# Optimization experiments

Hardware: AMD Instinct MI355X
Metric: run time of the kernel (lower is better)

The kernel has to match this reference:

```python
import jax, jax.numpy as jnp
import numpy as np

TOP_K = 2
ROUTED_SCALING = 1.0


def setup_inputs() -> dict:
    key = jax.random.key(0)
    k1, k2, k3, k4 = jax.random.split(key, 4)
    S, B, H = 1024, 2, 1024
    E, FFN = 8, 1408
    return {
        "hidden_states": jax.random.normal(k1, (S, B, H), dtype=jnp.float32),
        "gate_w": jax.random.normal(k2, (E, H), dtype=jnp.float32) * 0.02,
        "w1": jax.random.normal(k3, (E, H, 2 * FFN), dtype=jnp.float32) * 0.02,
        "w2": jax.random.normal(k4, (E, FFN, H), dtype=jnp.float32) * 0.02,
    }


def reference(hidden_states, gate_w, w1, w2):
    # hidden_states: [S, B, H] -> transpose(0,1) as in MoELayer.forward
    x = jnp.transpose(hidden_states, (1, 0, 2))  # [B, S, H]
    B, S, H = x.shape
    E = gate_w.shape[0]
    xt = x.reshape(-1, H)  # [T, H], T = B*S
    T = xt.shape[0]

    # --- TopKGate ('greedy', softmax scoring) ---
    scores = jax.nn.softmax(xt @ gate_w.T, axis=-1)  # [T, E]
    topk_w, topk_idx = jax.lax.top_k(scores, TOP_K)  # [T, K]
    # norm_topk_prob: normalize the top-k weights
    topk_w = topk_w / (jnp.sum(topk_w, axis=-1, keepdims=True) + 1e-20)
    topk_w = topk_w * ROUTED_SCALING

    # Sparse combine weights [T, E] (zero for non-selected experts)
    combine = jnp.zeros((T, E), dtype=xt.dtype)
    combine = combine.at[jnp.arange(T)[:, None], topk_idx].set(topk_w)

    # --- Experts: per-expert swiglu MLP, weighted combine ---
    # Equivalent math to dispatch -> per-expert grouped GEMM -> combine:
    # non-selected experts contribute with weight 0.
    out = jnp.zeros_like(xt)
    for e in range(E):
        h = xt @ w1[e]                      # [T, 2*FFN]
        g, u = jnp.split(h, 2, axis=-1)
        y = (jax.nn.silu(g) * u) @ w2[e]    # [T, H]
        out = out + combine[:, e:e + 1] * y

    out = out.reshape(B, S, H)
    return jnp.transpose(out, (1, 0, 2))  # back to [S, B, H]
```

## Files before the change

### kernel.cpp

```cpp
#include <hip/hip_runtime.h>
#include <hip/hip_bf16.h>

#define S_      1024
#define B_      2
#define H_      1024
#define E_      8
#define FFN_    1408
#define TWO_FFN 2816
#define T_      2048
#define MAXSLOTS 5120
#define NB_T1   (44 * 16 * 8)
#define NB_T2   (16 * 22 * 8)
#define NB_CONV 512
#define NB_PREP (NB_T1 + NB_T2 + NB_CONV)

typedef float  f32x4 __attribute__((ext_vector_type(4)));
typedef short  s16x8 __attribute__((ext_vector_type(8)));

__device__ __forceinline__ unsigned short f2bf(float f) {
    unsigned u = __float_as_uint(f);
    u += 0x7fffu + ((u >> 16) & 1u);
    return (unsigned short)(u >> 16);
}
__device__ __forceinline__ void async16(const void* g, void* l) {
    __builtin_amdgcn_global_load_lds(
        (const __attribute__((address_space(1))) unsigned int*)(unsigned long long)g,
        (__attribute__((address_space(3))) unsigned int*)(unsigned long long)l,
        16, 0, 0);
}
__device__ __forceinline__ size_t xrow_off(int t) {
    return (size_t)(t & (S_ - 1)) * (B_ * H_) + (size_t)(t >> 10) * H_;
}

__device__ __forceinline__ void transpose_body(const float* __restrict__ ip,
                                               unsigned short* __restrict__ op,
                                               int R, int C, int r0, int c0,
                                               float (*lds)[65], int tid) {
    int q = tid & 15, rr = tid >> 4;
#pragma unroll
    for (int i = 0; i < 4; i++) {
        int r = rr + 16 * i;
        const float4 v = *(const float4*)(ip + (size_t)(r0 + r) * C + c0 + q * 4);
        lds[q * 4 + 0][r] = v.x;
        lds[q * 4 + 1][r] = v.y;
        lds[q * 4 + 2][r] = v.z;
        lds[q * 4 + 3][r] = v.w;
    }
    __syncthreads();
    int oq = tid & 7, cc = tid >> 3;
#pragma unroll
    for (int i = 0; i < 2; i++) {
        int c = cc + 32 * i;
        const float* row = &lds[c][oq * 8];
        unsigned short o[8];
#pragma unroll
        for (int j = 0; j < 8; j++) o[j] = f2bf(row[j]);
        *(uint4*)(op + (size_t)(c0 + c) * R + r0 + oq * 8) = *(const uint4*)o;
    }
}

__global__ void k_prep(const float* __restrict__ hs, const float* __restrict__ gw,
                       const float* __restrict__ w1, const float* __restrict__ w2,
                       unsigned short* __restrict__ xb,
                       unsigned short* __restrict__ w1bt, unsigned short* __restrict__ w2bt,
                       int* __restrict__ topkI, float* __restrict__ topkW) {
    __shared__ float tile[64][65];
    int bx = blockIdx.x, tid = threadIdx.x;
    if (bx < NB_T1) {
        int e = bx / (44 * 16), rem = bx % (44 * 16);
        int c0 = (rem % 44) * 64, r0 = (rem / 44) * 64;
        transpose_body(w1 + (size_t)e * (H_ * TWO_FFN), w1bt + (size_t)e * (H_ * TWO_FFN),
                       H_, TWO_FFN, r0, c0, tile, tid);
        return;
    }
    if (bx < NB_T1 + NB_T2) {
        int b2 = bx - NB_T1;
        int e = b2 / (16 * 22), rem = b2 % (16 * 22);
        int c0 = (rem % 16) * 64, r0 = (rem / 16) * 64;
        transpose_body(w2 + (size_t)e * (FFN_ * H_), w2bt + (size_t)e * (FFN_ * H_),
                       FFN_, H_, r0, c0, tile, tid);
        return;
    }
    int cb = bx - (NB_T1 + NB_T2);
    int wid = tid >> 6, lane = tid & 63;
    int t = cb * 4 + wid;
    const float* xr = hs + xrow_off(t);
    unsigned short* xo = xb + (size_t)t * H_;
    float acc[E_];
#pragma unroll
    for (int e = 0; e < E_; e++) acc[e] = 0.f;
#pragma unroll
    for (int p = 0; p < 4; p++) {
        int h = p * 256 + lane * 4;
        const float4 v = *(const float4*)(xr + h);
        unsigned short o[4] = { f2bf(v.x), f2bf(v.y), f2bf(v.z), f2bf(v.w) };
        *(uint2*)(xo + h) = *(const uint2*)o;
#pragma unroll
        for (int e = 0; e < E_; e++) {
            const float4 g = *(const float4*)(gw + e * H_ + h);
            acc[e] += v.x * g.x + v.y * g.y + v.z * g.z + v.w * g.w;
        }
    }
#pragma unroll
    for (int e = 0; e < E_; e++)
        for (int off = 32; off > 0; off >>= 1) acc[e] += __shfl_down(acc[e], off);
    if (lane == 0) {
        float l0 = -1e30f, l1 = -1e30f; int i0 = 0, i1 = 0;
#pragma unroll
        for (int e = 0; e < E_; e++) {
            float v = acc[e];
            if (v > l0)      { l1 = l0; i1 = i0; l0 = v; i0 = e; }
            else if (v > l1) { l1 = v;  i1 = e; }
        }
        float p1 = expf(l1 - l0);
        float w0 = 1.f / (1.f + p1);
        float w1s = 1.f - w0;
        topkI[2 * t] = i0; topkI[2 * t + 1] = i1;
        topkW[2 * t] = w0; topkW[2 * t + 1] = w1s;
    }
}

__global__ void k_routeassign(const int* __restrict__ topkI, const float* __restrict__ topkW,
                              int* __restrict__ ctrl, int* __restrict__ perm,
                              int* __restrict__ slotOfTok) {
    __shared__ int s_wcnt[4][E_];
    __shared__ int s_base[E_];
    __shared__ int s_cur[E_];
    int tid = threadIdx.x, wid = tid >> 6, lane = tid & 63;
    int cnt[E_];
#pragma unroll
    for (int j = 0; j < E_; j++) cnt[j] = 0;
    for (int i = tid; i < 2 * T_; i += 256) {
        int e = topkI[i];
#pragma unroll
        for (int j = 0; j < E_; j++) cnt[j] += (e == j);
    }
#pragma unroll
    for (int j = 0; j < E_; j++)
        for (int off = 32; off > 0; off >>= 1) cnt[j] += __shfl_down(cnt[j], off);
    if (lane == 0) {
#pragma unroll
        for (int j = 0; j < E_; j++) s_wcnt[wid][j] = cnt[j];
    }
    __syncthreads();
    if (tid == 0) {
        int b = 0;
        for (int e = 0; e < E_; e++) {
            int n = s_wcnt[0][e] + s_wcnt[1][e] + s_wcnt[2][e] + s_wcnt[3][e];
            int ntile = (n + 127) >> 7;
            s_base[e] = b;
            ctrl[40 + e] = ntile;
            ctrl[48 + e] = b;
            b += ntile * 128;
        }
#pragma unroll
        for (int e = 0; e < E_; e++) s_cur[e] = 0;
    }
    __syncthreads();
    for (int s = tid; s < MAXSLOTS; s += 256) perm[s] = 0;
    __syncthreads();
    for (int t = tid; t < T_; t += 256) {
#pragma unroll
        for (int k = 0; k < 2; k++) {
            int e = topkI[2 * t + k];
            int pos = atomicAdd(&s_cur[e], 1);
            int slot = s_base[e] + pos;
            perm[slot] = t;
            slotOfTok[2 * t + k] = slot;
        }
    }
}

__global__ __launch_bounds__(256) void k_gemm1(
    const unsigned short* __restrict__ xb, const unsigned short* __restrict__ w1bt,
    const int* __restrict__ ctrl, const int* __restrict__ perm,
    unsigned short* __restrict__ A2) {
    int e  = blockIdx.x & 7;
    int ct = blockIdx.x >> 3;
    int ti = blockIdx.y;
    if (ti >= ctrl[40 + e]) return;
    int slot0 = ctrl[48 + e] + ti * 128;
    __shared__ __align__(16) unsigned short smem[2 * 128 * 64];
    unsigned short* As = smem;
    unsigned short* Bs = smem + 128 * 64;
    int tid = threadIdx.x, wid = tid >> 6, lane = tid & 63;

    const unsigned short* aPtr[4];
    const unsigned short* bPtr[4];
    unsigned short* lA[4];
    unsigned short* lB[4];
#pragma unroll
    for (int i = 0; i < 4; i++) {
        int c = (wid * 4 + i) * 64 + lane;
        int r = c >> 3;
        int qd = (c & 7) ^ (r & 7);
        int col8 = qd * 8;
        int tok = perm[slot0 + r];
        int gr = (r < 64) ? (ct * 64 + r) : (FFN_ + ct * 64 + (r - 64));
        aPtr[i] = xb + (size_t)tok * H_ + col8;
        bPtr[i] = w1bt + ((size_t)e * TWO_FFN + gr) * H_ + col8;
        lA[i] = As + (size_t)c * 8;
        lB[i] = Bs + (size_t)c * 8;
    }
    f32x4 acc[4][4];
#pragma unroll
    for (int mi = 0; mi < 4; mi++)
#pragma unroll
        for (int ni = 0; ni < 4; ni++) acc[mi][ni] = (f32x4){0.f, 0.f, 0.f, 0.f};
    int wm = wid & 1, wn = wid >> 1;
    int rowB = wm * 64, colB = wn * 64;
    int sw = (lane & 7) << 3;

    for (int k0 = 0; k0 < H_; k0 += 64) {
#pragma unroll
        for (int i = 0; i < 4; i++) { async16(aPtr[i] + k0, lA[i]); async16(bPtr[i] + k0, lB[i]); }
        __syncthreads();
#pragma unroll
        for (int kk = 0; kk < 64; kk += 32) {
            int kr = (kk + ((lane >> 4) << 3)) ^ sw;
            s16x8 af[4], bf[4];
#pragma unroll
            for (int mi = 0; mi < 4; mi++) af[mi] = *(const s16x8*)&As[(rowB + mi * 16 + (lane & 15)) * 64 + kr];
#pragma unroll
            for (int ni = 0; ni < 4; ni++) bf[ni] = *(const s16x8*)&Bs[(colB + ni * 16 + (lane & 15)) * 64 + kr];
#pragma unroll
            for (int mi = 0; mi < 4; mi++)
#pragma unroll
                for (int ni = 0; ni < 4; ni++)
                    acc[mi][ni] = __builtin_amdgcn_mfma_f32_16x16x32_bf16(af[mi], bf[ni], acc[mi][ni], 0, 0, 0);
        }
        __syncthreads();
    }
    float* upLds = (float*)smem;
    if (wn == 1) {
#pragma unroll
        for (int mi = 0; mi < 4; mi++)
#pragma unroll
            for (int ni = 0; ni < 4; ni++)
#pragma unroll
                for (int r = 0; r < 4; r++) {
                    int m = rowB + mi * 16 + (lane >> 4) * 4 + r;
                    int u = ni * 16 + (lane & 15);
                    upLds[m * 64 + u] = acc[mi][ni][r];
                }
    }
    __syncthreads();
    if (wn == 0) {
#pragma unroll
        for (int mi = 0; mi < 4; mi++)
#pragma unroll
            for (int r = 0; r < 4; r++) {
                int m = rowB + mi * 16 + (lane >> 4) * 4 + r;
                unsigned short* arow = A2 + (size_t)(slot0 + m) * FFN_ + ct * 64;
#pragma unroll
                for (int ni = 0; ni < 4; ni++) {
                    int gl = ni * 16 + (lane & 15);
                    float g = acc[mi][ni][r];
                    float u = upLds[m * 64 + gl];
                    float s = g / (1.f + expf(-g));
                    arow[gl] = f2bf(s * u);
                }
            }
    }
}

__global__ __launch_bounds__(256) void k_gemm2(
    const unsigned short* __restrict__ A2, const unsigned short* __restrict__ w2bt,
    const int* __restrict__ ctrl, unsigned short* __restrict__ Yp) {
    int e  = blockIdx.x & 7;
    int ct = blockIdx.x >> 3;
    int ti = blockIdx.y;
    if (ti >= ctrl[40 + e]) return;
    int slot0 = ctrl[48 + e] + ti * 128;
    int ks    = blockIdx.z;
    __shared__ __align__(16) unsigned short As[128 * 64];
    __shared__ __align__(16) unsigned short Bs[128 * 64];
    int tid = threadIdx.x, wid = tid >> 6, lane = tid & 63;

    const unsigned short* aPtr[4];
    const unsigned short* bPtr[4];
    unsigned short* lA[4];
    unsigned short* lB[4];
#pragma unroll
    for (int i = 0; i < 4; i++) {
        int c = (wid * 4 + i) * 64 + lane;
        int r = c >> 3;
        int qd = (c & 7) ^ (r & 7);
        int col8 = qd * 8;
        aPtr[i] = A2 + (size_t)(slot0 + r) * FFN_ + col8;
        bPtr[i] = w2bt + ((size_t)e * H_ + ct * 128 + r) * FFN_ + col8;
        lA[i] = As + (size_t)c * 8;
        lB[i] = Bs + (size_t)c * 8;
    }
    f32x4 acc[4][4];
#pragma unroll
    for (int mi = 0; mi < 4; mi++)
#pragma unroll
        for (int ni = 0; ni < 4; ni++) acc[mi][ni] = (f32x4){0.f, 0.f, 0.f, 0.f};
    int wm = wid & 1, wn = wid >> 1;
    int rowB = wm * 64, colB = wn * 64;
    int sw = (lane & 7) << 3;

    int kbeg = ks * (FFN_ / 2), kend = kbeg + FFN_ / 2;
    for (int k0 = kbeg; k0 < kend; k0 += 64) {
#pragma unroll
        for (int i = 0; i < 4; i++) { async16(aPtr[i] + k0, lA[i]); async16(bPtr[i] + k0, lB[i]); }
        __syncthreads();
#pragma unroll
        for (int kk = 0; kk < 64; kk += 32) {
            int kr = (kk + ((lane >> 4) << 3)) ^ sw;
            s16x8 af[4], bf[4];
#pragma unroll
            for (int mi = 0; mi < 4; mi++) af[mi] = *(const s16x8*)&As[(rowB + mi * 16 + (lane & 15)) * 64 + kr];
#pragma unroll
            for (int ni = 0; ni < 4; ni++) bf[ni] = *(const s16x8*)&Bs[(colB + ni * 16 + (lane & 15)) * 64 + kr];
#pragma unroll
            for (int mi = 0; mi < 4; mi++)
#pragma unroll
                for (int ni = 0; ni < 4; ni++)
                    acc[mi][ni] = __builtin_amdgcn_mfma_f32_16x16x32_bf16(af[mi], bf[ni], acc[mi][ni], 0, 0, 0);
        }
        __syncthreads();
    }
    unsigned short* yp = Yp + (size_t)ks * MAXSLOTS * H_;
#pragma unroll
    for (int mi = 0; mi < 4; mi++)
#pragma unroll
        for (int r = 0; r < 4; r++) {
            int m = rowB + mi * 16 + (lane >> 4) * 4 + r;
#pragma unroll
            for (int ni = 0; ni < 4; ni++) {
                int n = colB + ni * 16 + (lane & 15);
                yp[(size_t)(slot0 + m) * H_ + ct * 128 + n] = f2bf(acc[mi][ni][r]);
            }
        }
}

__global__ void k_combine(const unsigned short* __restrict__ Yp, const int* __restrict__ slotOfTok,
                          const float* __restrict__ topkW, float* __restrict__ out) {
    int t = blockIdx.x;
    int h = threadIdx.x * 4;
    int sA = slotOfTok[2 * t], sB = slotOfTok[2 * t + 1];
    float wA = topkW[2 * t],   wB = topkW[2 * t + 1];
    const unsigned short* pA0 = Yp + (size_t)sA * H_ + h;
    const unsigned short* pA1 = Yp + ((size_t)MAXSLOTS + sA) * H_ + h;
    const unsigned short* pB0 = Yp + (size_t)sB * H_ + h;
    const unsigned short* pB1 = Yp + ((size_t)MAXSLOTS + sB) * H_ + h;
    unsigned short a0[4], a1[4], b0[4], b1[4];
    *(uint2*)a0 = *(const uint2*)pA0;
    *(uint2*)a1 = *(const uint2*)pA1;
    *(uint2*)b0 = *(const uint2*)pB0;
    *(uint2*)b1 = *(const uint2*)pB1;
    float4 r;
    float* rp = (float*)&r;
#pragma unroll
    for (int i = 0; i < 4; i++) {
        float av = __uint_as_float(((unsigned)a0[i]) << 16) + __uint_as_float(((unsigned)a1[i]) << 16);
        float bv = __uint_as_float(((unsigned)b0[i]) << 16) + __uint_as_float(((unsigned)b1[i]) << 16);
        rp[i] = wA * av + wB * bv;
    }
    *(float4*)(out + xrow_off(t) + h) = r;
}

extern "C" void kernel_launch(void* const* d_in, const int* in_sizes, int n_in,
                              void* d_out, int out_size, void* d_ws, size_t ws_size,
                              hipStream_t stream) {
    (void)in_sizes; (void)n_in; (void)ws_size; (void)out_size;
    const float* hs = (const float*)d_in[0];
    const float* gw = (const float*)d_in[1];
    const float* w1 = (const float*)d_in[2];
    const float* w2 = (const float*)d_in[3];
    float* out = (float*)d_out;
    char* ws = (char*)d_ws;

    int*            ctrl   = (int*)ws;
    int*            topkI  = (int*)(ws + (16u << 10));
    float*          topkW  = (float*)(ws + (48u << 10));
    int*            perm   = (int*)(ws + (80u << 10));
    int*            slotOfTok = (int*)(ws + (144u << 10));
    unsigned short* xb    = (unsigned short*)(ws + (1ull  << 20));
    unsigned short* w1bt  = (unsigned short*)(ws + (5ull  << 20));
    unsigned short* Yp    = (unsigned short*)(ws + (5ull << 20));
    unsigned short* w2bt  = (unsigned short*)(ws + (49ull << 20));
    unsigned short* A2    = (unsigned short*)(ws + (71ull << 20));

    k_prep<<<NB_PREP, 256, 0, stream>>>(hs, gw, w1, w2, xb, w1bt, w2bt, topkI, topkW);
    k_routeassign<<<1, 256, 0, stream>>>(topkI, topkW, ctrl, perm, slotOfTok);
    k_gemm1<<<dim3(8 * (FFN_ / 64), 16), 256, 0, stream>>>(xb, w1bt, ctrl, perm, A2);
    k_gemm2<<<dim3(8 * (H_ / 128), 16, 2), 256, 0, stream>>>(A2, w2bt, ctrl, Yp);
    k_combine<<<2048, 256, 0, stream>>>(Yp, slotOfTok, topkW, out);
}
```

Before: 274.8 us.

## Fuse combine into GEMM2 via atomics, overlap w2 transpose with GEMM1

The w2 transpose moves out of the prep kernel into extra blocks of the GEMM1 launch, so it runs alongside the first expert GEMM. Each transpose block now handles 8 tiles with register double-buffering of the loads. GEMM2 drops its split-K partial outputs and the separate combine kernel. It uses smaller 128x32 tiles and atomically adds routing-weighted results straight into a zeroed fp32 output. This removes the bf16 Yp round-trip and one launch, but adds a memset, float atomics with nondeterministic summation order, and smaller tiles that reread A2 more often.

New measurement: 275.8 us. About the same (+0.4%).

```diff
diff --git a/kernel.cpp b/kernel.cpp
--- a/kernel.cpp
+++ b/kernel.cpp
@@ -9,10 +9,10 @@
 #define TWO_FFN 2816
 #define T_      2048
 #define MAXSLOTS 5120
-#define NB_T1   (44 * 16 * 8)
-#define NB_T2   (16 * 22 * 8)
+
+#define NB_T1   704
 #define NB_CONV 512
-#define NB_PREP (NB_T1 + NB_T2 + NB_CONV)
+#define NB_PREP (NB_T1 + NB_CONV)
 
 typedef float  f32x4 __attribute__((ext_vector_type(4)));
 typedef short  s16x8 __attribute__((ext_vector_type(8)));
@@ -32,21 +32,26 @@
     return (size_t)(t & (S_ - 1)) * (B_ * H_) + (size_t)(t >> 10) * H_;
 }
 
-__device__ __forceinline__ void transpose_body(const float* __restrict__ ip,
-                                               unsigned short* __restrict__ op,
-                                               int R, int C, int r0, int c0,
-                                               float (*lds)[65], int tid) {
+__device__ __forceinline__ void tp_load(const float* __restrict__ ip, int C,
+                                        int r0, int c0, int tid, float4* v) {
+    int q = tid & 15, rr = tid >> 4;
+#pragma unroll
+    for (int i = 0; i < 4; i++)
+        v[i] = *(const float4*)(ip + (size_t)(r0 + rr + 16 * i) * C + c0 + q * 4);
+}
+__device__ __forceinline__ void tp_to_lds(const float4* v, float (*lds)[65], int tid) {
     int q = tid & 15, rr = tid >> 4;
 #pragma unroll
     for (int i = 0; i < 4; i++) {
         int r = rr + 16 * i;
-        const float4 v = *(const float4*)(ip + (size_t)(r0 + r) * C + c0 + q * 4);
-        lds[q * 4 + 0][r] = v.x;
-        lds[q * 4 + 1][r] = v.y;
-        lds[q * 4 + 2][r] = v.z;
-        lds[q * 4 + 3][r] = v.w;
-    }
-    __syncthreads();
+        lds[q * 4 + 0][r] = v[i].x;
+        lds[q * 4 + 1][r] = v[i].y;
+        lds[q * 4 + 2][r] = v[i].z;
+        lds[q * 4 + 3][r] = v[i].w;
+    }
+}
+__device__ __forceinline__ void tp_store(unsigned short* __restrict__ op, int R,
+                                         int r0, int c0, float (*lds)[65], int tid) {
     int oq = tid & 7, cc = tid >> 3;
 #pragma unroll
     for (int i = 0; i < 2; i++) {
@@ -59,29 +64,39 @@
     }
 }
 
-__global__ void k_prep(const float* __restrict__ hs, const float* __restrict__ gw,
-                       const float* __restrict__ w1, const float* __restrict__ w2,
-                       unsigned short* __restrict__ xb,
-                       unsigned short* __restrict__ w1bt, unsigned short* __restrict__ w2bt,
-                       int* __restrict__ topkI, float* __restrict__ topkW) {
+__global__ __launch_bounds__(256) void k_prep(
+    const float* __restrict__ hs, const float* __restrict__ gw,
+    const float* __restrict__ w1,
+    unsigned short* __restrict__ xb, unsigned short* __restrict__ w1bt,
+    int* __restrict__ topkI, float* __restrict__ topkW) {
     __shared__ float tile[64][65];
     int bx = blockIdx.x, tid = threadIdx.x;
     if (bx < NB_T1) {
-        int e = bx / (44 * 16), rem = bx % (44 * 16);
+        float4 cur[4], nxt[4];
+        int idx = bx * 8;
+        int e = idx / 704, rem = idx % 704;
         int c0 = (rem % 44) * 64, r0 = (rem / 44) * 64;
-        transpose_body(w1 + (size_t)e * (H_ * TWO_FFN), w1bt + (size_t)e * (H_ * TWO_FFN),
-                       H_, TWO_FFN, r0, c0, tile, tid);
+        tp_load(w1 + (size_t)e * (H_ * TWO_FFN), TWO_FFN, r0, c0, tid, cur);
+#pragma unroll
+        for (int s = 0; s < 8; s++) {
+            tp_to_lds(cur, tile, tid);
+            __syncthreads();
+            int e2 = 0, c2 = 0, r2 = 0;
+            if (s < 7) {
+                int idx2 = idx + s + 1;
+                e2 = idx2 / 704; int rm2 = idx2 % 704;
+                c2 = (rm2 % 44) * 64; r2 = (rm2 / 44) * 64;
+                tp_load(w1 + (size_t)e2 * (H_ * TWO_FFN), TWO_FFN, r2, c2, tid, nxt);
+            }
+            tp_store(w1bt + (size_t)e * (H_ * TWO_FFN), H_, r0, c0, tile, tid);
+            __syncthreads();
+            e = e2; c0 = c2; r0 = r2;
+#pragma unroll
+            for (int i = 0; i < 4; i++) cur[i] = nxt[i];
+        }
         return;
     }
-    if (bx < NB_T1 + NB_T2) {
-        int b2 = bx - NB_T1;
-        int e = b2 / (16 * 22), rem = b2 % (16 * 22);
-        int c0 = (rem % 16) * 64, r0 = (rem / 16) * 64;
-        transpose_body(w2 + (size_t)e * (FFN_ * H_), w2bt + (size_t)e * (FFN_ * H_),
-                       FFN_, H_, r0, c0, tile, tid);
-        return;
-    }
-    int cb = bx - (NB_T1 + NB_T2);
+    int cb = bx - NB_T1;
     int wid = tid >> 6, lane = tid & 63;
     int t = cb * 4 + wid;
     const float* xr = hs + xrow_off(t);
@@ -122,15 +137,15 @@
 
 __global__ void k_routeassign(const int* __restrict__ topkI, const float* __restrict__ topkW,
                               int* __restrict__ ctrl, int* __restrict__ perm,
-                              int* __restrict__ slotOfTok) {
-    __shared__ int s_wcnt[4][E_];
+                              float* __restrict__ wgt) {
+    __shared__ int s_wcnt[16][E_];
     __shared__ int s_base[E_];
     __shared__ int s_cur[E_];
     int tid = threadIdx.x, wid = tid >> 6, lane = tid & 63;
     int cnt[E_];
 #pragma unroll
     for (int j = 0; j < E_; j++) cnt[j] = 0;
-    for (int i = tid; i < 2 * T_; i += 256) {
+    for (int i = tid; i < 2 * T_; i += 1024) {
         int e = topkI[i];
 #pragma unroll
         for (int j = 0; j < E_; j++) cnt[j] += (e == j);
@@ -146,7 +161,8 @@
     if (tid == 0) {
         int b = 0;
         for (int e = 0; e < E_; e++) {
-            int n = s_wcnt[0][e] + s_wcnt[1][e] + s_wcnt[2][e] + s_wcnt[3][e];
+            int n = 0;
+            for (int w = 0; w < 16; w++) n += s_wcnt[w][e];
             int ntile = (n + 127) >> 7;
             s_base[e] = b;
             ctrl[40 + e] = ntile;
@@ -157,33 +173,62 @@
         for (int e = 0; e < E_; e++) s_cur[e] = 0;
     }
     __syncthreads();
-    for (int s = tid; s < MAXSLOTS; s += 256) perm[s] = 0;
+    for (int s = tid; s < MAXSLOTS; s += 1024) { perm[s] = 0; wgt[s] = 0.f; }
     __syncthreads();
-    for (int t = tid; t < T_; t += 256) {
+    for (int t = tid; t < T_; t += 1024) {
 #pragma unroll
         for (int k = 0; k < 2; k++) {
             int e = topkI[2 * t + k];
             int pos = atomicAdd(&s_cur[e], 1);
             int slot = s_base[e] + pos;
             perm[slot] = t;
-            slotOfTok[2 * t + k] = slot;
-        }
-    }
-}
-
-__global__ __launch_bounds__(256) void k_gemm1(
+            wgt[slot]  = topkW[2 * t + k];
+        }
+    }
+}
+
+__global__ __launch_bounds__(256) void k_gemm1x(
     const unsigned short* __restrict__ xb, const unsigned short* __restrict__ w1bt,
+    const float* __restrict__ w2, unsigned short* __restrict__ w2bt,
     const int* __restrict__ ctrl, const int* __restrict__ perm,
     unsigned short* __restrict__ A2) {
+    __shared__ __align__(16) unsigned short smem[2 * 128 * 64];
+    int tid = threadIdx.x;
+    if (blockIdx.y >= 16) {
+        float (*tile)[65] = (float(*)[65])smem;
+        int tb = blockIdx.x + 176 * (blockIdx.y - 16);
+        float4 cur[4], nxt[4];
+        int idx = tb * 8;
+        int e = idx / 352, rem = idx % 352;
+        int c0 = (rem & 15) * 64, r0 = (rem >> 4) * 64;
+        tp_load(w2 + (size_t)e * (FFN_ * H_), H_, r0, c0, tid, cur);
+#pragma unroll
+        for (int s = 0; s < 8; s++) {
+            tp_to_lds(cur, tile, tid);
+            __syncthreads();
+            int e2 = 0, c2 = 0, r2 = 0;
+            if (s < 7) {
+                int idx2 = idx + s + 1;
+                e2 = idx2 / 352; int rm2 = idx2 % 352;
+                c2 = (rm2 & 15) * 64; r2 = (rm2 >> 4) * 64;
+                tp_load(w2 + (size_t)e2 * (FFN_ * H_), H_, r2, c2, tid, nxt);
+            }
+            tp_store(w2bt + (size_t)e * (FFN_ * H_), FFN_, r0, c0, tile, tid);
+            __syncthreads();
+            e = e2; c0 = c2; r0 = r2;
+#pragma unroll
+            for (int i = 0; i < 4; i++) cur[i] = nxt[i];
+        }
+        return;
+    }
     int e  = blockIdx.x & 7;
     int ct = blockIdx.x >> 3;
     int ti = blockIdx.y;
     if (ti >= ctrl[40 + e]) return;
     int slot0 = ctrl[48 + e] + ti * 128;
-    __shared__ __align__(16) unsigned short smem[2 * 128 * 64];
     unsigned short* As = smem;
     unsigned short* Bs = smem + 128 * 64;
-    int tid = threadIdx.x, wid = tid >> 6, lane = tid & 63;
+    int wid = tid >> 6, lane = tid & 63;
 
     const unsigned short* aPtr[4];
     const unsigned short* bPtr[4];
@@ -264,108 +309,84 @@
     }
 }
 
-__global__ __launch_bounds__(256) void k_gemm2(
+__global__ __launch_bounds__(256) void k_gemm2f(
     const unsigned short* __restrict__ A2, const unsigned short* __restrict__ w2bt,
-    const int* __restrict__ ctrl, unsigned short* __restrict__ Yp) {
-    int e  = blockIdx.x & 7;
-    int ct = blockIdx.x >> 3;
-    int ti = blockIdx.y;
+    const int* __restrict__ ctrl, const int* __restrict__ perm,
+    const float* __restrict__ wgt, float* __restrict__ out) {
+    int e   = blockIdx.x & 7;
+    int hct = blockIdx.x >> 3;
+    int ti  = blockIdx.y;
     if (ti >= ctrl[40 + e]) return;
     int slot0 = ctrl[48 + e] + ti * 128;
-    int ks    = blockIdx.z;
     __shared__ __align__(16) unsigned short As[128 * 64];
-    __shared__ __align__(16) unsigned short Bs[128 * 64];
+    __shared__ __align__(16) unsigned short Bs[32 * 64];
     int tid = threadIdx.x, wid = tid >> 6, lane = tid & 63;
 
     const unsigned short* aPtr[4];
-    const unsigned short* bPtr[4];
     unsigned short* lA[4];
-    unsigned short* lB[4];
 #pragma unroll
     for (int i = 0; i < 4; i++) {
         int c = (wid * 4 + i) * 64 + lane;
         int r = c >> 3;
-        int qd = (c & 7) ^ (r & 7);
-        int col8 = qd * 8;
+        int col8 = ((c & 7) ^ (r & 7)) * 8;
         aPtr[i] = A2 + (size_t)(slot0 + r) * FFN_ + col8;
-        bPtr[i] = w2bt + ((size_t)e * H_ + ct * 128 + r) * FFN_ + col8;
         lA[i] = As + (size_t)c * 8;
-        lB[i] = Bs + (size_t)c * 8;
-    }
-    f32x4 acc[4][4];
-#pragma unroll
-    for (int mi = 0; mi < 4; mi++)
-#pragma unroll
-        for (int ni = 0; ni < 4; ni++) acc[mi][ni] = (f32x4){0.f, 0.f, 0.f, 0.f};
-    int wm = wid & 1, wn = wid >> 1;
-    int rowB = wm * 64, colB = wn * 64;
+    }
+    int cB = tid, rB2 = cB >> 3;
+    int colB8 = ((cB & 7) ^ (rB2 & 7)) * 8;
+    const unsigned short* bPtr = w2bt + ((size_t)e * H_ + hct * 32 + rB2) * FFN_ + colB8;
+    unsigned short* lB = Bs + (size_t)cB * 8;
+
+    f32x4 acc[2][2];
+#pragma unroll
+    for (int mi = 0; mi < 2; mi++)
+#pragma unroll
+        for (int ni = 0; ni < 2; ni++) acc[mi][ni] = (f32x4){0.f, 0.f, 0.f, 0.f};
+    int rowB = wid * 32;
     int sw = (lane & 7) << 3;
 
-    int kbeg = ks * (FFN_ / 2), kend = kbeg + FFN_ / 2;
-    for (int k0 = kbeg; k0 < kend; k0 += 64) {
-#pragma unroll
-        for (int i = 0; i < 4; i++) { async16(aPtr[i] + k0, lA[i]); async16(bPtr[i] + k0, lB[i]); }
+    for (int k0 = 0; k0 < FFN_; k0 += 64) {
+#pragma unroll
+        for (int i = 0; i < 4; i++) async16(aPtr[i] + k0, lA[i]);
+        async16(bPtr + k0, lB);
         __syncthreads();
 #pragma unroll
         for (int kk = 0; kk < 64; kk += 32) {
             int kr = (kk + ((lane >> 4) << 3)) ^ sw;
-            s16x8 af[4], bf[4];
-#pragma unroll
-            for (int mi = 0; mi < 4; mi++) af[mi] = *(const s16x8*)&As[(rowB + mi * 16 + (lane & 15)) * 64 + kr];
-#pragma unroll
-            for (int ni = 0; ni < 4; ni++) bf[ni] = *(const s16x8*)&Bs[(colB + ni * 16 + (lane & 15)) * 64 + kr];
-#pragma unroll
-            for (int mi = 0; mi < 4; mi++)
-#pragma unroll
-                for (int ni = 0; ni < 4; ni++)
+            s16x8 af[2], bf[2];
+#pragma unroll
+            for (int mi = 0; mi < 2; mi++) af[mi] = *(const s16x8*)&As[(rowB + mi * 16 + (lane & 15)) * 64 + kr];
+#pragma unroll
+            for (int ni = 0; ni < 2; ni++) bf[ni] = *(const s16x8*)&Bs[(ni * 16 + (lane & 15)) * 64 + kr];
+#pragma unroll
+            for (int mi = 0; mi < 2; mi++)
+#pragma unroll
+                for (int ni = 0; ni < 2; ni++)
                     acc[mi][ni] = __builtin_amdgcn_mfma_f32_16x16x32_bf16(af[mi], bf[ni], acc[mi][ni], 0, 0, 0);
         }
         __syncthreads();
     }
-    unsigned short* yp = Yp + (size_t)ks * MAXSLOTS * H_;
-#pragma unroll
-    for (int mi = 0; mi < 4; mi++)
+#pragma unroll
+    for (int mi = 0; mi < 2; mi++)
 #pragma unroll
         for (int r = 0; r < 4; r++) {
             int m = rowB + mi * 16 + (lane >> 4) * 4 + r;
-#pragma unroll
-            for (int ni = 0; ni < 4; ni++) {
-                int n = colB + ni * 16 + (lane & 15);
-                yp[(size_t)(slot0 + m) * H_ + ct * 128 + n] = f2bf(acc[mi][ni][r]);
+            int slot = slot0 + m;
+            float wv = wgt[slot];
+            if (wv != 0.f) {
+                int tok = perm[slot];
+                float* orow = out + xrow_off(tok) + hct * 32;
+#pragma unroll
+                for (int ni = 0; ni < 2; ni++)
+                    atomicAdd(&orow[ni * 16 + (lane & 15)], wv * acc[mi][ni][r]);
             }
         }
-}
-
-__global__ void k_combine(const unsigned short* __restrict__ Yp, const int* __restrict__ slotOfTok,
-                          const float* __restrict__ topkW, float* __restrict__ out) {
-    int t = blockIdx.x;
-    int h = threadIdx.x * 4;
-    int sA = slotOfTok[2 * t], sB = slotOfTok[2 * t + 1];
-    float wA = topkW[2 * t],   wB = topkW[2 * t + 1];
-    const unsigned short* pA0 = Yp + (size_t)sA * H_ + h;
-    const unsigned short* pA1 = Yp + ((size_t)MAXSLOTS + sA) * H_ + h;
-    const unsigned short* pB0 = Yp + (size_t)sB * H_ + h;
-    const unsigned short* pB1 = Yp + ((size_t)MAXSLOTS + sB) * H_ + h;
-    unsigned short a0[4], a1[4], b0[4], b1[4];
-    *(uint2*)a0 = *(const uint2*)pA0;
-    *(uint2*)a1 = *(const uint2*)pA1;
-    *(uint2*)b0 = *(const uint2*)pB0;
-    *(uint2*)b1 = *(const uint2*)pB1;
-    float4 r;
-    float* rp = (float*)&r;
-#pragma unroll
-    for (int i = 0; i < 4; i++) {
-        float av = __uint_as_float(((unsigned)a0[i]) << 16) + __uint_as_float(((unsigned)a1[i]) << 16);
-        float bv = __uint_as_float(((unsigned)b0[i]) << 16) + __uint_as_float(((unsigned)b1[i]) << 16);
-        rp[i] = wA * av + wB * bv;
-    }
-    *(float4*)(out + xrow_off(t) + h) = r;
 }
 
 extern "C" void kernel_launch(void* const* d_in, const int* in_sizes, int n_in,
                               void* d_out, int out_size, void* d_ws, size_t ws_size,
                               hipStream_t stream) {
-    (void)in_sizes; (void)n_in; (void)ws_size; (void)out_size;
+    (void)in_sizes; (void)n_in; (void)ws_size;
     const float* hs = (const float*)d_in[0];
     const float* gw = (const float*)d_in[1];
     const float* w1 = (const float*)d_in[2];
@@ -373,20 +394,19 @@
     float* out = (float*)d_out;
     char* ws = (char*)d_ws;
 
-    int*            ctrl   = (int*)ws;
-    int*            topkI  = (int*)(ws + (16u << 10));
-    float*          topkW  = (float*)(ws + (48u << 10));
-    int*            perm   = (int*)(ws + (80u << 10));
-    int*            slotOfTok = (int*)(ws + (144u << 10));
+    int*            ctrl  = (int*)ws;
+    int*            topkI = (int*)(ws + (16u << 10));
+    float*          topkW = (float*)(ws + (48u << 10));
+    int*            perm  = (int*)(ws + (80u << 10));
+    float*          wgt   = (float*)(ws + (112u << 10));
     unsigned short* xb    = (unsigned short*)(ws + (1ull  << 20));
     unsigned short* w1bt  = (unsigned short*)(ws + (5ull  << 20));
-    unsigned short* Yp    = (unsigned short*)(ws + (5ull << 20));
     unsigned short* w2bt  = (unsigned short*)(ws + (49ull << 20));
     unsigned short* A2    = (unsigned short*)(ws + (71ull << 20));
 
-    k_prep<<<NB_PREP, 256, 0, stream>>>(hs, gw, w1, w2, xb, w1bt, w2bt, topkI, topkW);
-    k_routeassign<<<1, 256, 0, stream>>>(topkI, topkW, ctrl, perm, slotOfTok);
-    k_gemm1<<<dim3(8 * (FFN_ / 64), 16), 256, 0, stream>>>(xb, w1bt, ctrl, perm, A2);
-    k_gemm2<<<dim3(8 * (H_ / 128), 16, 2), 256, 0, stream>>>(A2, w2bt, ctrl, Yp);
-    k_combine<<<2048, 256, 0, stream>>>(Yp, slotOfTok, topkW, out);
-}
+    hipMemsetAsync(out, 0, (size_t)out_size * sizeof(float), stream);
+    k_prep<<<NB_PREP, 256, 0, stream>>>(hs, gw, w1, xb, w1bt, topkI, topkW);
+    k_routeassign<<<1, 1024, 0, stream>>>(topkI, topkW, ctrl, perm, wgt);
+    k_gemm1x<<<dim3(176, 18), 256, 0, stream>>>(xb, w1bt, w2, w2bt, ctrl, perm, A2);
+    k_gemm2f<<<dim3(256, 16), 256, 0, stream>>>(A2, w2bt, ctrl, perm, wgt, out);
+}
```
